# Performance work log

Hardware: AMD Instinct MI355X
Metric: run time of the kernel (lower is better)

## Reference

```python
import jax, jax.numpy as jnp
import numpy as np

NEG_SLOPE = 0.2  # PyG GATConv default


def gat_layer(x, src, dst, W, att_src, att_dst, bias, num_nodes):
    """One PyG-style GATConv (concat=True, add_self_loops handled by caller).
    x: [N, F_in], W: [F_in, H*C], att_src/att_dst: [H, C], bias: [H*C].
    """
    H, C = att_src.shape
    h = (x @ W).reshape(num_nodes, H, C)              # [N, H, C]
    a_src = (h * att_src).sum(-1)                     # [N, H]
    a_dst = (h * att_dst).sum(-1)                     # [N, H]
    e = jax.nn.leaky_relu(a_src[src] + a_dst[dst], NEG_SLOPE)  # [E, H]
    # segment softmax over destination neighborhoods
    m = jax.ops.segment_max(e, dst, num_segments=num_nodes)   # [N, H]
    ex = jnp.exp(e - m[dst])
    denom = jax.ops.segment_sum(ex, dst, num_segments=num_nodes)
    alpha = ex / denom[dst]                           # [E, H]
    out = jax.ops.segment_sum(alpha[:, :, None] * h[src], dst,
                              num_segments=num_nodes)  # [N, H, C]
    return out.reshape(num_nodes, H * C) + bias


def setup_inputs() -> dict:
    key = jax.random.key(0)
    ks = jax.random.split(key, 12)
    N, E, D, H = 50000, 800000, 128, 8
    C = D // H
    x = jax.random.normal(ks[0], (N, D), dtype=jnp.float32)
    edge_index = jax.random.randint(ks[1], (2, E), 0, N, dtype=jnp.int64)
    s = 0.1
    return {
        "x": x,
        "edge_index": edge_index,
        "W1": s * jax.random.normal(ks[2], (D, H * C), dtype=jnp.float32),
        "as1": s * jax.random.normal(ks[3], (H, C), dtype=jnp.float32),
        "ad1": s * jax.random.normal(ks[4], (H, C), dtype=jnp.float32),
        "b1": jnp.zeros((H * C,), dtype=jnp.float32),
        "W2": s * jax.random.normal(ks[5], (D, H * C), dtype=jnp.float32),
        "as2": s * jax.random.normal(ks[6], (H, C), dtype=jnp.float32),
        "ad2": s * jax.random.normal(ks[7], (H, C), dtype=jnp.float32),
        "b2": jnp.zeros((H * C,), dtype=jnp.float32),
    }


def reference(x, edge_index, W1, as1, ad1, b1, W2, as2, ad2, b2):
    n = x.shape[0]
    # PyG GATConv default add_self_loops=True
    loop = jnp.arange(n, dtype=edge_index.dtype)
    src = jnp.concatenate([edge_index[0], loop])
    dst = jnp.concatenate([edge_index[1], loop])
    h = jax.nn.relu(gat_layer(x, src, dst, W1, as1, ad1, b1, n))
    # dropout p=0.5 is identity in eval mode
    return gat_layer(h, src, dst, W2, as2, ad2, b2, n)
```

## Files before the change

kernel.cpp:

```cpp
#include <hip/hip_runtime.h>
#include <math.h>

#define D 128
#define H 8
#define C 16
#define NEG_SLOPE 0.2f
#define SCAN_TILE 1024

#define BSHIFT 12
#define BRANGE 4096
#define NBMAX 16
#define EPT 32
#define BEDGES (256 * EPT)
#define CAP 98304
#define NSEG 16

typedef unsigned short ushortT;
typedef __attribute__((ext_vector_type(8))) short short8;
typedef __attribute__((ext_vector_type(4))) float f32x4;

__device__ __forceinline__ float bf2f(unsigned short v) {
    union { unsigned int i; float f; } c;
    c.i = ((unsigned int)v) << 16;
    return c.f;
}
__device__ __forceinline__ unsigned short f2bf(float f) {
    union { float f; unsigned int i; } c;
    c.f = f;
    unsigned int lsb = (c.i >> 16) & 1u;
    c.i += 0x7fffu + lsb;
    return (unsigned short)(c.i >> 16);
}

__device__ __forceinline__ int padc(int c) { return (c + 4) & ~3; }



__device__ __forceinline__ void bucket_part(
    int b, int t, const int* __restrict__ ei, int* __restrict__ bkt,
    int* __restrict__ bcur, int E) {
    __shared__ int wtot[4][NBMAX];
    __shared__ int wbase[4][NBMAX];
    int w = t >> 6, lane = t & 63;
    int base = b * BEDGES;

    int cnt[NBMAX];
#pragma unroll
    for (int q = 0; q < NBMAX; q++) cnt[q] = 0;

#pragma unroll
    for (int it = 0; it < EPT / 4; it++) {
        int idx = base + it * 1024 + t * 4;
        if (idx + 3 < E) {
            int4 dv = *(const int4*)(ei + (size_t)E + idx);
            int b0 = dv.x >> BSHIFT, b1 = dv.y >> BSHIFT;
            int b2 = dv.z >> BSHIFT, b3 = dv.w >> BSHIFT;
#pragma unroll
            for (int q = 0; q < NBMAX; q++)
                cnt[q] += (b0 == q) + (b1 == q) + (b2 == q) + (b3 == q);
        } else {
            for (int k = idx; k < E && k < idx + 4; k++) {
                int bq = ei[(size_t)E + k] >> BSHIFT;
#pragma unroll
                for (int q = 0; q < NBMAX; q++) cnt[q] += (bq == q);
            }
        }
    }

    int pre[NBMAX];
#pragma unroll
    for (int q = 0; q < NBMAX; q++) {
        int p = cnt[q];
#pragma unroll
        for (int o = 1; o < 64; o <<= 1) {
            int v = __shfl_up(p, o);
            if (lane >= o) p += v;
        }
        pre[q] = p - cnt[q];
        if (lane == 63) wtot[w][q] = p;
    }
    __syncthreads();
    if (t < NBMAX) {
        int q = t;
        int s0 = wtot[0][q], s1 = wtot[1][q], s2 = wtot[2][q], s3 = wtot[3][q];
        int tot = s0 + s1 + s2 + s3;
        int gb = (tot > 0) ? atomicAdd(bcur + q * 16, tot) : 0;
        wbase[0][q] = gb;
        wbase[1][q] = gb + s0;
        wbase[2][q] = gb + s0 + s1;
        wbase[3][q] = gb + s0 + s1 + s2;
    }
    __syncthreads();
    int cur[NBMAX];
#pragma unroll
    for (int q = 0; q < NBMAX; q++) cur[q] = wbase[w][q] + pre[q];

#pragma unroll
    for (int it = 0; it < EPT / 4; it++) {
        int idx = base + it * 1024 + t * 4;
        if (idx + 3 < E) {
            int4 sv = *(const int4*)(ei + idx);
            int4 dv = *(const int4*)(ei + (size_t)E + idx);
            int dd[4] = {dv.x, dv.y, dv.z, dv.w};
            int ss[4] = {sv.x, sv.y, sv.z, sv.w};
#pragma unroll
            for (int e = 0; e < 4; e++) {
                int bq = dd[e] >> BSHIFT;
                int pk = ((dd[e] & (BRANGE - 1)) << 17) | ss[e];
                int off = cur[0];
#pragma unroll
                for (int q = 1; q < NBMAX; q++) off = (bq == q) ? cur[q] : off;
                if (off < CAP) bkt[(size_t)bq * CAP + off] = pk;
#pragma unroll
                for (int q = 0; q < NBMAX; q++) cur[q] += (bq == q);
            }
        } else {
            for (int k = idx; k < E && k < idx + 4; k++) {
                int d = ei[(size_t)E + k], s = ei[k];
                int bq = d >> BSHIFT;
                int pk = ((d & (BRANGE - 1)) << 17) | s;
                int off = cur[0];
#pragma unroll
                for (int q = 1; q < NBMAX; q++) off = (bq == q) ? cur[q] : off;
                if (off < CAP) bkt[(size_t)bq * CAP + off] = pk;
#pragma unroll
                for (int q = 0; q < NBMAX; q++) cur[q] += (bq == q);
            }
        }
    }
}

__device__ __forceinline__ void wprep_part(
    int b2, int t, const float* __restrict__ W1, const float* __restrict__ as1,
    const float* __restrict__ ad1, const float* __restrict__ W2,
    const float* __restrict__ as2, const float* __restrict__ ad2,
    ushortT* __restrict__ wf1_hi, ushortT* __restrict__ wf1_lo,
    ushortT* __restrict__ wf2_hi, ushortT* __restrict__ wf2_lo) {
    const float *W, *att_s, *att_d;
    ushortT *whi, *wlo;
    int idx;
    if (b2 < 9) {
        W = W1; att_s = as1; att_d = ad1; whi = wf1_hi; wlo = wf1_lo;
        idx = b2 * 256 + t;
    } else {
        W = W2; att_s = as2; att_d = ad2; whi = wf2_hi; wlo = wf2_lo;
        idx = (b2 - 9) * 256 + t;
    }
    if (idx >= 4 * 9 * 64) return;
    int lane = idx & 63;
    int nt = (idx >> 6) % 9;
    int kt = idx / (9 * 64);
    int quad = lane >> 4, ncol = lane & 15;
#pragma unroll
    for (int j = 0; j < 8; j++) {
        int k = kt * 32 + quad * 8 + j;
        float v;
        if (nt < 8) {
            v = W[k * D + nt * 16 + ncol];
        } else {
            const float* att = (ncol < 8) ? att_s : att_d;
            int hd = ncol & 7;
            float s = 0.f;
            for (int c = 0; c < 16; c++)
                s += W[k * D + hd * 16 + c] * att[hd * 16 + c];
            v = s;
        }
        unsigned short hi = f2bf(v);
        unsigned short lo = f2bf(v - bf2f(hi));
        whi[idx * 8 + j] = hi;
        wlo[idx * 8 + j] = lo;
    }
}

__device__ __forceinline__ void xsplit_part(
    int idx, const float* __restrict__ x, ushortT* __restrict__ xh,
    ushortT* __restrict__ xl, int n, int nt16) {
    int r = idx >> 4;
    if (r >= nt16 * 16) return;
    int kb = idx & 15;
    float4 v0 = make_float4(0.f, 0.f, 0.f, 0.f), v1 = v0;
    if (r < n) {
        v0 = ((const float4*)(x + (size_t)r * D + kb * 8))[0];
        v1 = ((const float4*)(x + (size_t)r * D + kb * 8))[1];
    }
    int wt = r >> 4, m = r & 15, kt = kb >> 2, quad = kb & 3;
    int base = ((wt * 4 + kt) * 64 + (m + 16 * quad)) * 8;
    ushort4 h0, l0, h1, l1;
    h0.x = f2bf(v0.x); l0.x = f2bf(v0.x - bf2f(h0.x));
    h0.y = f2bf(v0.y); l0.y = f2bf(v0.y - bf2f(h0.y));
    h0.z = f2bf(v0.z); l0.z = f2bf(v0.z - bf2f(h0.z));
    h0.w = f2bf(v0.w); l0.w = f2bf(v0.w - bf2f(h0.w));
    h1.x = f2bf(v1.x); l1.x = f2bf(v1.x - bf2f(h1.x));
    h1.y = f2bf(v1.y); l1.y = f2bf(v1.y - bf2f(h1.y));
    h1.z = f2bf(v1.z); l1.z = f2bf(v1.z - bf2f(h1.z));
    h1.w = f2bf(v1.w); l1.w = f2bf(v1.w - bf2f(h1.w));
    *(ushort4*)(xh + base) = h0;
    *(ushort4*)(xh + base + 4) = h1;
    *(ushort4*)(xl + base) = l0;
    *(ushort4*)(xl + base + 4) = l1;
}

__global__ __launch_bounds__(256) void k_prep(
    const int* __restrict__ ei, int* __restrict__ bkt, int* __restrict__ bcur,
    int E, const float* __restrict__ x, ushortT* __restrict__ xh,
    ushortT* __restrict__ xl, int n, int nt16,
    const float* __restrict__ W1, const float* __restrict__ as1,
    const float* __restrict__ ad1, const float* __restrict__ W2,
    const float* __restrict__ as2, const float* __restrict__ ad2,
    ushortT* __restrict__ wf1_hi, ushortT* __restrict__ wf1_lo,
    ushortT* __restrict__ wf2_hi, ushortT* __restrict__ wf2_lo, int nbb) {
    int b = blockIdx.x;
    int t = threadIdx.x;
    if (b < nbb) {
        bucket_part(b, t, ei, bkt, bcur, E);
    } else if (b < nbb + 18) {
        wprep_part(b - nbb, t, W1, as1, ad1, W2, as2, ad2,
                   wf1_hi, wf1_lo, wf2_hi, wf2_lo);
    } else {
        xsplit_part((b - nbb - 18) * 256 + t, x, xh, xl, n, nt16);
    }
}


__global__ __launch_bounds__(256) void k_count(
    const int* __restrict__ bkt, const int* __restrict__ bcur,
    int* __restrict__ hseg, int n) {
    __shared__ int lcnt[BRANGE];
    int t = threadIdx.x;
    int q = blockIdx.x >> 4, s = blockIdx.x & (NSEG - 1);
    for (int i = t; i < BRANGE; i += 256) lcnt[i] = 0;
    __syncthreads();
    int tot = bcur[q * 16];
    if (tot > CAP) tot = CAP;
    int per = ((tot + NSEG - 1) / NSEG + 3) & ~3;
    int lo = s * per;
    int hi = lo + per; if (hi > tot) hi = tot;
    const int* bp = bkt + (size_t)q * CAP;
    for (int i = lo + t * 4; i < hi; i += 1024) {
        if (i + 3 < hi) {
            int4 v = *(const int4*)(bp + i);
            atomicAdd(&lcnt[v.x >> 17], 1);
            atomicAdd(&lcnt[v.y >> 17], 1);
            atomicAdd(&lcnt[v.z >> 17], 1);
            atomicAdd(&lcnt[v.w >> 17], 1);
        } else {
            for (int k = i; k < hi; k++) atomicAdd(&lcnt[bp[k] >> 17], 1);
        }
    }
    __syncthreads();
    int* hp = hseg + ((size_t)(q * NSEG + s) << BSHIFT);
    for (int i = t; i < BRANGE; i += 256) hp[i] = lcnt[i];
}


__global__ __launch_bounds__(256) void k_scan_lb(
    int* __restrict__ hseg, int* __restrict__ poffs,
    int* __restrict__ sstate, int* __restrict__ csrsrc, int n) {
    __shared__ int lds[256];
    __shared__ int bprefix;
    int t = threadIdx.x;
    int b = blockIdx.x;
    int base = b * SCAN_TILE + t * 4;
    int q = base >> BSHIFT;
    int li = base & (BRANGE - 1);
    int4 hv[NSEG];
    int c[4] = {0, 0, 0, 0};
    bool any = (base < n);
    if (any) {
#pragma unroll
        for (int s = 0; s < NSEG; s++) {
            hv[s] = *(const int4*)(hseg + ((size_t)(q * NSEG + s) << BSHIFT) + li);
            c[0] += hv[s].x; c[1] += hv[s].y; c[2] += hv[s].z; c[3] += hv[s].w;
        }
    }
    int ssum = padc(c[0]) + padc(c[1]) + padc(c[2]) + padc(c[3]);
    lds[t] = ssum;
    __syncthreads();
    for (int st = 1; st < 256; st <<= 1) {
        int add = (t >= st) ? lds[t - st] : 0;
        __syncthreads();
        lds[t] += add;
        __syncthreads();
    }
    if (t == 0)
        __hip_atomic_store(&sstate[b], lds[255] | (1 << 30),
                           __ATOMIC_RELEASE, __HIP_MEMORY_SCOPE_AGENT);
    if (t < 64) {
        int v = 0;
        if (t < b) {
            int x;
            do {
                x = __hip_atomic_load(&sstate[t], __ATOMIC_RELAXED,
                                      __HIP_MEMORY_SCOPE_AGENT);
            } while (!(x & (1 << 30)));
            v = x & 0x3FFFFFFF;
        }
#pragma unroll
        for (int o = 32; o > 0; o >>= 1) v += __shfl_down(v, o);
        if (t == 0) bprefix = v;
    }
    __syncthreads();
    int run = bprefix + ((t == 0) ? 0 : lds[t - 1]);
    if (b == 0 && t == 0) poffs[0] = 0;
    int runk[4];
#pragma unroll
    for (int k = 0; k < 4; k++) {
        int i = base + k;
        runk[k] = run;
        if (i < n) {
            int pv = padc(c[k]);
            csrsrc[run + c[k]] = i;
            for (int k2 = c[k] + 1; k2 < pv; k2++)
                csrsrc[run + k2] = n;
            run += pv;
            poffs[i + 1] = run;
        }
    }
    if (any) {
        int a0 = runk[0], a1 = runk[1], a2 = runk[2], a3 = runk[3];
#pragma unroll
        for (int s = 0; s < NSEG; s++) {
            int4 v = hv[s];
            int4 w; w.x = a0; w.y = a1; w.z = a2; w.w = a3;
            *(int4*)(hseg + ((size_t)(q * NSEG + s) << BSHIFT) + li) = w;
            a0 += v.x; a1 += v.y; a2 += v.z; a3 += v.w;
        }
    }
}


__device__ __forceinline__ void gemm_wave(
    int wt, int lane, const ushortT* __restrict__ xh,
    const ushortT* __restrict__ xl, const ushortT* __restrict__ wf_hi,
    const ushortT* __restrict__ wf_lo, ushortT* __restrict__ hout,
    float* __restrict__ as_, float* __restrict__ ad_, int n) {
    f32x4 acc[9];
#pragma unroll
    for (int nt = 0; nt < 9; nt++) acc[nt] = (f32x4){0.f, 0.f, 0.f, 0.f};

#pragma unroll
    for (int kt = 0; kt < 4; kt++) {
        short8 a_hi = *(const short8*)(xh + (size_t)((wt * 4 + kt) * 64 + lane) * 8);
        short8 a_lo = *(const short8*)(xl + (size_t)((wt * 4 + kt) * 64 + lane) * 8);
        const ushortT* bh = wf_hi + (size_t)(kt * 576 + lane) * 8;
        const ushortT* bl = wf_lo + (size_t)(kt * 576 + lane) * 8;
#pragma unroll
        for (int nt = 0; nt < 9; nt++) {
            short8 b_hi = *(const short8*)(bh + nt * 512);
            short8 b_lo = *(const short8*)(bl + nt * 512);
            acc[nt] = __builtin_amdgcn_mfma_f32_16x16x32_bf16(a_hi, b_hi, acc[nt], 0, 0, 0);
            acc[nt] = __builtin_amdgcn_mfma_f32_16x16x32_bf16(a_lo, b_hi, acc[nt], 0, 0, 0);
            acc[nt] = __builtin_amdgcn_mfma_f32_16x16x32_bf16(a_hi, b_lo, acc[nt], 0, 0, 0);
        }
    }

    int q = lane >> 4, ncol = lane & 15;
    int rbase = wt * 16 + q * 4;
#pragma unroll
    for (int nt = 0; nt < 8; nt++) {
#pragma unroll
        for (int reg = 0; reg < 4; reg++) {
            int r = rbase + reg;
            if (r < n) hout[(size_t)r * D + nt * 16 + ncol] = f2bf(acc[nt][reg]);
        }
    }
#pragma unroll
    for (int reg = 0; reg < 4; reg++) {
        int r = rbase + reg;
        if (r < n) {
            float v = acc[8][reg];
            if (ncol < 8) as_[r * H + ncol] = v;
            else          ad_[r * H + (ncol - 8)] = v;
        }
    }
}


__global__ __launch_bounds__(256) void k_fillgemm(
    const int* __restrict__ poffs, const int* __restrict__ bkt,
    const int* __restrict__ bcur, const int* __restrict__ hseg,
    int* __restrict__ csrsrc,
    ushortT* __restrict__ hbuf_s, float* __restrict__ asrc_s,
    const ushortT* __restrict__ xh, const ushortT* __restrict__ xl,
    const ushortT* __restrict__ wf_hi, const ushortT* __restrict__ wf_lo,
    ushortT* __restrict__ hout, float* __restrict__ as_,
    float* __restrict__ ad_, int n, int gb, int nrb) {
    int b = blockIdx.x;
    int t = threadIdx.x;
    if (b < gb) {
        int wt = b * 4 + (t >> 6);
        if (wt * 16 < n)
            gemm_wave(wt, t & 63, xh, xl, wf_hi, wf_lo, hout, as_, ad_, n);
        return;
    }
    int rb = b - gb;
    if (rb < nrb) {
        __shared__ int cur[BRANGE];
        int q = rb >> 4, s = rb & (NSEG - 1);
        const int* sp = hseg + ((size_t)(q * NSEG + s) << BSHIFT);
        for (int i = t; i < BRANGE; i += 256) cur[i] = sp[i];
        __syncthreads();
        int tot = bcur[q * 16];
        if (tot > CAP) tot = CAP;
        int per = ((tot + NSEG - 1) / NSEG + 3) & ~3;
        int lo = s * per;
        int hi = lo + per; if (hi > tot) hi = tot;
        const int* bp = bkt + (size_t)q * CAP;
        for (int i = lo + t * 4; i < hi; i += 1024) {
            if (i + 3 < hi) {
                int4 v = *(const int4*)(bp + i);
                int s0 = atomicAdd(&cur[v.x >> 17], 1);
                int s1 = atomicAdd(&cur[v.y >> 17], 1);
                int s2 = atomicAdd(&cur[v.z >> 17], 1);
                int s3 = atomicAdd(&cur[v.w >> 17], 1);
                csrsrc[s0] = v.x & 0x1FFFF;
                csrsrc[s1] = v.y & 0x1FFFF;
                csrsrc[s2] = v.z & 0x1FFFF;
                csrsrc[s3] = v.w & 0x1FFFF;
            } else {
                for (int k = i; k < hi; k++) {
                    int v = bp[k];
                    int sl = atomicAdd(&cur[v >> 17], 1);
                    csrsrc[sl] = v & 0x1FFFF;
                }
            }
        }
        return;
    }
    if (rb == nrb && t == 0) {
        int total = poffs[n];
        for (int k = 0; k < 8; k++) csrsrc[total + k] = n;
        for (int k = 0; k < D; k++) hbuf_s[(size_t)n * D + k] = 0;
        for (int h = 0; h < H; h++) asrc_s[n * H + h] = -1e30f;
    }
}


__global__ __launch_bounds__(256) void k_gemm_att(
    const ushortT* __restrict__ xh, const ushortT* __restrict__ xl,
    const ushortT* __restrict__ wf_hi, const ushortT* __restrict__ wf_lo,
    ushortT* __restrict__ hout, float* __restrict__ as_,
    float* __restrict__ ad_, int n) {
    int t = threadIdx.x;
    int wt = blockIdx.x * 4 + (t >> 6);
    if (wt * 16 >= n) return;
    gemm_wave(wt, t & 63, xh, xl, wf_hi, wf_lo, hout, as_, ad_, n);
}


__global__ __launch_bounds__(256) void k_aggregate(
    const ushortT* __restrict__ hbuf, const float* __restrict__ asrc,
    const float* __restrict__ adst, const int* __restrict__ csr,
    const int* __restrict__ poffs, const float* __restrict__ bias,
    float* __restrict__ out, ushortT* __restrict__ oh, ushortT* __restrict__ ol,
    int out_mode, int n) {
    int t = threadIdx.x;
    int d = blockIdx.x * 8 + (t >> 5);
    if (d >= n) return;
    int ll = t & 31;
    int h = ll >> 2;
    int llo = ll * 2;
    const unsigned int* hb = (const unsigned int*)hbuf;

    int off = poffs[d];
    int degp = poffs[d + 1] - off;
    float adh = adst[d * H + h];
    const int* cp = csr + off;

    f32x4 acc = {0.f, 0.f, 0.f, 0.f};
    float ssum = 0.f;

    int j = 0;
    for (; j + 8 <= degp; j += 8) {
        int4 sa = *(const int4*)(cp + j);
        int4 sb = *(const int4*)(cp + j + 4);
        int s_[8] = {sa.x, sa.y, sa.z, sa.w, sb.x, sb.y, sb.z, sb.w};
        float e_[8];
        uint2 u_[8];
#pragma unroll
        for (int k = 0; k < 8; k++) {
            e_[k] = asrc[s_[k] * H + h];
            u_[k] = *(const uint2*)(hb + s_[k] * 64 + llo);
        }
#pragma unroll
        for (int k = 0; k < 8; k++) {
            float e = e_[k] + adh;
            float w = __expf(fmaxf(e, NEG_SLOPE * e));
            ssum += w;
            f32x4 hv;
            hv.x = __uint_as_float(u_[k].x << 16);
            hv.y = __uint_as_float(u_[k].x & 0xffff0000u);
            hv.z = __uint_as_float(u_[k].y << 16);
            hv.w = __uint_as_float(u_[k].y & 0xffff0000u);
            acc += hv * w;
        }
    }
    if (j < degp) {
        int4 sa = *(const int4*)(cp + j);
        int s_[4] = {sa.x, sa.y, sa.z, sa.w};
        float e_[4];
        uint2 u_[4];
#pragma unroll
        for (int k = 0; k < 4; k++) {
            e_[k] = asrc[s_[k] * H + h];
            u_[k] = *(const uint2*)(hb + s_[k] * 64 + llo);
        }
#pragma unroll
        for (int k = 0; k < 4; k++) {
            float e = e_[k] + adh;
            float w = __expf(fmaxf(e, NEG_SLOPE * e));
            ssum += w;
            f32x4 hv;
            hv.x = __uint_as_float(u_[k].x << 16);
            hv.y = __uint_as_float(u_[k].x & 0xffff0000u);
            hv.z = __uint_as_float(u_[k].y << 16);
            hv.w = __uint_as_float(u_[k].y & 0xffff0000u);
            acc += hv * w;
        }
    }

    float inv = 1.f / ssum;
    float4 b = ((const float4*)bias)[ll];
    float4 r;
    r.x = acc.x * inv + b.x;
    r.y = acc.y * inv + b.y;
    r.z = acc.z * inv + b.z;
    r.w = acc.w * inv + b.w;

    if (out_mode == 0) {
        ((float4*)(out + (size_t)d * D))[ll] = r;
    } else {
        r.x = fmaxf(r.x, 0.f);
        r.y = fmaxf(r.y, 0.f);
        r.z = fmaxf(r.z, 0.f);
        r.w = fmaxf(r.w, 0.f);
        int wt = d >> 4, m = d & 15;
        int kt = ll >> 3, quad = (ll >> 1) & 3, j0 = (ll & 1) * 4;
        int base = ((wt * 4 + kt) * 64 + (m + 16 * quad)) * 8 + j0;
        ushort4 hv, lv;
        hv.x = f2bf(r.x); lv.x = f2bf(r.x - bf2f(hv.x));
        hv.y = f2bf(r.y); lv.y = f2bf(r.y - bf2f(hv.y));
        hv.z = f2bf(r.z); lv.z = f2bf(r.z - bf2f(hv.z));
        hv.w = f2bf(r.w); lv.w = f2bf(r.w - bf2f(hv.w));
        *(ushort4*)(oh + base) = hv;
        *(ushort4*)(ol + base) = lv;
    }
}


extern "C" void kernel_launch(void* const* d_in, const int* in_sizes, int n_in,
                              void* d_out, int out_size, void* d_ws, size_t ws_size,
                              hipStream_t stream) {
    const float* x   = (const float*)d_in[0];
    const int*   ei  = (const int*)d_in[1];
    const float* W1  = (const float*)d_in[2];
    const float* as1 = (const float*)d_in[3];
    const float* ad1 = (const float*)d_in[4];
    const float* b1  = (const float*)d_in[5];
    const float* W2  = (const float*)d_in[6];
    const float* as2 = (const float*)d_in[7];
    const float* ad2 = (const float*)d_in[8];
    const float* b2  = (const float*)d_in[9];
    float* out = (float*)d_out;

    int N = in_sizes[0] / D;
    int E = in_sizes[1] / 2;
    int NT16 = (N + 15) / 16;
    int nb_scan = (N + SCAN_TILE - 1) / SCAN_TILE;
    int nbkt = (N + BRANGE - 1) >> BSHIFT;
    int nrb = nbkt * NSEG;
    const int WFN = 4 * 9 * 64 * 8;
    size_t XS = (size_t)NT16 * 2048;

    ushortT* hbuf = (ushortT*)d_ws;
    ushortT* xsh  = hbuf + (size_t)(N + 1) * D;
    ushortT* xsl  = xsh + XS;
    float* asrc = (float*)(xsl + XS);
    float* adst = asrc + (size_t)(N + 1) * H;
    int*   poffs  = (int*)(adst + (size_t)N * H);
    int*   sstate = poffs + ((N + 1 + 3) & ~3);
    int*   bcur   = sstate + 64;
    int*   csrsrc = bcur + 256;
    int*   bkt    = csrsrc + ((E + 4 * N + 8 + 3) & ~3);
    int*   hseg   = bkt + (size_t)nbkt * CAP;
    ushortT* wf1_hi = (ushortT*)(hseg + (size_t)nrb * BRANGE);
    ushortT* wf1_lo = wf1_hi + WFN;
    ushortT* wf2_hi = wf1_lo + WFN;
    ushortT* wf2_lo = wf2_hi + WFN;

    hipMemsetAsync(sstate, 0, 320 * sizeof(int), stream);

    int nbb = (E + BEDGES - 1) / BEDGES;
    int nbx = (NT16 * 16 * 16 + 255) / 256;
    k_prep<<<nbb + 18 + nbx, 256, 0, stream>>>(
        ei, bkt, bcur, E, x, xsh, xsl, N, NT16,
        W1, as1, ad1, W2, as2, ad2, wf1_hi, wf1_lo, wf2_hi, wf2_lo, nbb);

    k_count<<<nrb, 256, 0, stream>>>(bkt, bcur, hseg, N);

    k_scan_lb<<<nb_scan, 256, 0, stream>>>(hseg, poffs, sstate, csrsrc, N);

    int gb = (NT16 + 3) / 4;
    int ab = (N + 7) / 8;
    k_fillgemm<<<gb + nrb + 1, 256, 0, stream>>>(
        poffs, bkt, bcur, hseg, csrsrc, hbuf, asrc,
        xsh, xsl, wf1_hi, wf1_lo, hbuf, asrc, adst, N, gb, nrb);
    k_aggregate<<<ab, 256, 0, stream>>>(hbuf, asrc, adst, csrsrc, poffs, b1,
                                        out, xsh, xsl, 1, N);
    k_gemm_att<<<gb, 256, 0, stream>>>(xsh, xsl, wf2_hi, wf2_lo, hbuf, asrc, adst, N);
    k_aggregate<<<ab, 256, 0, stream>>>(hbuf, asrc, adst, csrsrc, poffs, b2,
                                        out, xsh, xsl, 0, N);
}
```

Baseline: 239.3 us.

## Fuse layer-1 aggregation with layer-2 GEMM using per-tile readiness flags

Merges the layer-1 aggregate kernel and the layer-2 GEMM kernel into one launch. GEMM waves spin on per-16-row-tile atomic counters that the aggregation blocks release once their rows are written, so GEMM work overlaps the tail of aggregation. A second set of h and a_src/a_dst buffers is added so the GEMM output does not overwrite data still being read by aggregation, and the counter array is zeroed by the existing memset. This removes one kernel boundary and its drain/launch gap. It relies on the producer blocks being scheduled before the spinning consumers, since lower block indices usually dispatch first, which risks deadlock or wasted slots if they are not.

```diff
diff --git a/kernel.cpp b/kernel.cpp
--- a/kernel.cpp
+++ b/kernel.cpp
@@ -381,6 +381,7 @@
     const int* __restrict__ bcur, const int* __restrict__ hseg,
     int* __restrict__ csrsrc,
     ushortT* __restrict__ hbuf_s, float* __restrict__ asrc_s,
+    ushortT* __restrict__ hbuf2_s, float* __restrict__ asrc2_s,
     const ushortT* __restrict__ xh, const ushortT* __restrict__ xl,
     const ushortT* __restrict__ wf_hi, const ushortT* __restrict__ wf_lo,
     ushortT* __restrict__ hout, float* __restrict__ as_,
@@ -430,34 +431,24 @@
     if (rb == nrb && t == 0) {
         int total = poffs[n];
         for (int k = 0; k < 8; k++) csrsrc[total + k] = n;
-        for (int k = 0; k < D; k++) hbuf_s[(size_t)n * D + k] = 0;
-        for (int h = 0; h < H; h++) asrc_s[n * H + h] = -1e30f;
-    }
-}
-
-
-__global__ __launch_bounds__(256) void k_gemm_att(
-    const ushortT* __restrict__ xh, const ushortT* __restrict__ xl,
-    const ushortT* __restrict__ wf_hi, const ushortT* __restrict__ wf_lo,
-    ushortT* __restrict__ hout, float* __restrict__ as_,
-    float* __restrict__ ad_, int n) {
-    int t = threadIdx.x;
-    int wt = blockIdx.x * 4 + (t >> 6);
-    if (wt * 16 >= n) return;
-    gemm_wave(wt, t & 63, xh, xl, wf_hi, wf_lo, hout, as_, ad_, n);
-}
-
-
-__global__ __launch_bounds__(256) void k_aggregate(
-    const ushortT* __restrict__ hbuf, const float* __restrict__ asrc,
-    const float* __restrict__ adst, const int* __restrict__ csr,
-    const int* __restrict__ poffs, const float* __restrict__ bias,
-    float* __restrict__ out, ushortT* __restrict__ oh, ushortT* __restrict__ ol,
-    int out_mode, int n) {
-    int t = threadIdx.x;
-    int d = blockIdx.x * 8 + (t >> 5);
-    if (d >= n) return;
-    int ll = t & 31;
+        for (int k = 0; k < D; k++) {
+            hbuf_s[(size_t)n * D + k] = 0;
+            hbuf2_s[(size_t)n * D + k] = 0;
+        }
+        for (int h = 0; h < H; h++) {
+            asrc_s[n * H + h] = -1e30f;
+            asrc2_s[n * H + h] = -1e30f;
+        }
+    }
+}
+
+
+__device__ __forceinline__ void agg_body(
+    int d, int ll, const ushortT* __restrict__ hbuf,
+    const float* __restrict__ asrc, const float* __restrict__ adst,
+    const int* __restrict__ csr, const int* __restrict__ poffs,
+    const float* __restrict__ bias, float* __restrict__ out,
+    ushortT* __restrict__ oh, ushortT* __restrict__ ol, int out_mode) {
     int h = ll >> 2;
     int llo = ll * 2;
     const unsigned int* hb = (const unsigned int*)hbuf;
@@ -548,6 +539,50 @@
 }
 
 
+__global__ __launch_bounds__(256) void k_aggregate(
+    const ushortT* __restrict__ hbuf, const float* __restrict__ asrc,
+    const float* __restrict__ adst, const int* __restrict__ csr,
+    const int* __restrict__ poffs, const float* __restrict__ bias,
+    float* __restrict__ out, int n) {
+    int t = threadIdx.x;
+    int d = blockIdx.x * 8 + (t >> 5);
+    if (d >= n) return;
+    agg_body(d, t & 31, hbuf, asrc, adst, csr, poffs, bias, out,
+             (ushortT*)nullptr, (ushortT*)nullptr, 0);
+}
+
+
+__global__ __launch_bounds__(256) void k_agg_gemm(
+    const ushortT* __restrict__ hbuf, const float* __restrict__ asrc,
+    const float* __restrict__ adst, const int* __restrict__ csr,
+    const int* __restrict__ poffs, const float* __restrict__ bias,
+    ushortT* __restrict__ oh, ushortT* __restrict__ ol,
+    const ushortT* __restrict__ wf_hi, const ushortT* __restrict__ wf_lo,
+    ushortT* __restrict__ hout2, float* __restrict__ as2,
+    float* __restrict__ ad2, int* __restrict__ tready, int n, int ab) {
+    int b = blockIdx.x;
+    int t = threadIdx.x;
+    if (b < ab) {
+        int d = b * 8 + (t >> 5);
+        if (d < n)
+            agg_body(d, t & 31, hbuf, asrc, adst, csr, poffs, bias,
+                     (float*)nullptr, oh, ol, 1);
+        __syncthreads();
+        if (t == 0)
+            __hip_atomic_fetch_add(&tready[b >> 1], 1, __ATOMIC_RELEASE,
+                                   __HIP_MEMORY_SCOPE_AGENT);
+        return;
+    }
+    int wt = (b - ab) * 4 + (t >> 6);
+    if (wt * 16 >= n) return;
+    int need = (wt * 2 + 2 <= ab) ? 2 : 1;
+    while (__hip_atomic_load(&tready[wt], __ATOMIC_ACQUIRE,
+                             __HIP_MEMORY_SCOPE_AGENT) < need)
+        __builtin_amdgcn_s_sleep(8);
+    gemm_wave(wt, t & 63, oh, ol, wf_hi, wf_lo, hout2, as2, ad2, n);
+}
+
+
 extern "C" void kernel_launch(void* const* d_in, const int* in_sizes, int n_in,
                               void* d_out, int out_size, void* d_ws, size_t ws_size,
                               hipStream_t stream) {
@@ -572,15 +607,19 @@
     const int WFN = 4 * 9 * 64 * 8;
     size_t XS = (size_t)NT16 * 2048;
 
-    ushortT* hbuf = (ushortT*)d_ws;
-    ushortT* xsh  = hbuf + (size_t)(N + 1) * D;
-    ushortT* xsl  = xsh + XS;
-    float* asrc = (float*)(xsl + XS);
-    float* adst = asrc + (size_t)(N + 1) * H;
-    int*   poffs  = (int*)(adst + (size_t)N * H);
+    ushortT* hbuf  = (ushortT*)d_ws;
+    ushortT* hbuf2 = hbuf + (size_t)(N + 1) * D;
+    ushortT* xsh   = hbuf2 + (size_t)(N + 1) * D;
+    ushortT* xsl   = xsh + XS;
+    float* asrc  = (float*)(xsl + XS);
+    float* asrc2 = asrc + (size_t)(N + 1) * H;
+    float* adst  = asrc2 + (size_t)(N + 1) * H;
+    float* adst2 = adst + (size_t)N * H;
+    int*   poffs  = (int*)(adst2 + (size_t)N * H);
     int*   sstate = poffs + ((N + 1 + 3) & ~3);
     int*   bcur   = sstate + 64;
-    int*   csrsrc = bcur + 256;
+    int*   tready = bcur + 256;
+    int*   csrsrc = tready + ((NT16 + 3) & ~3);
     int*   bkt    = csrsrc + ((E + 4 * N + 8 + 3) & ~3);
     int*   hseg   = bkt + (size_t)nbkt * CAP;
     ushortT* wf1_hi = (ushortT*)(hseg + (size_t)nrb * BRANGE);
@@ -588,7 +627,8 @@
     ushortT* wf2_hi = wf1_lo + WFN;
     ushortT* wf2_lo = wf2_hi + WFN;
 
-    hipMemsetAsync(sstate, 0, 320 * sizeof(int), stream);
+    hipMemsetAsync(sstate, 0,
+                   (size_t)(64 + 256 + ((NT16 + 3) & ~3)) * sizeof(int), stream);
 
     int nbb = (E + BEDGES - 1) / BEDGES;
     int nbx = (NT16 * 16 * 16 + 255) / 256;
@@ -603,11 +643,11 @@
     int gb = (NT16 + 3) / 4;
     int ab = (N + 7) / 8;
     k_fillgemm<<<gb + nrb + 1, 256, 0, stream>>>(
-        poffs, bkt, bcur, hseg, csrsrc, hbuf, asrc,
+        poffs, bkt, bcur, hseg, csrsrc, hbuf, asrc, hbuf2, asrc2,
         xsh, xsl, wf1_hi, wf1_lo, hbuf, asrc, adst, N, gb, nrb);
-    k_aggregate<<<ab, 256, 0, stream>>>(hbuf, asrc, adst, csrsrc, poffs, b1,
-                                        out, xsh, xsl, 1, N);
-    k_gemm_att<<<gb, 256, 0, stream>>>(xsh, xsl, wf2_hi, wf2_lo, hbuf, asrc, adst, N);
-    k_aggregate<<<ab, 256, 0, stream>>>(hbuf, asrc, adst, csrsrc, poffs, b2,
-                                        out, xsh, xsl, 0, N);
-}
+    k_agg_gemm<<<ab + gb, 256, 0, stream>>>(
+        hbuf, asrc, adst, csrsrc, poffs, b1, xsh, xsl,
+        wf2_hi, wf2_lo, hbuf2, asrc2, adst2, tready, N, ab);
+    k_aggregate<<<ab, 256, 0, stream>>>(hbuf2, asrc2, adst2, csrsrc, poffs, b2,
+                                        out, N);
+}
```

After: 448.4 us. +87.4%, slower.
